# Kernel tuning notes

Hardware: AMD Instinct MI355X
Metric: run time of the kernel (lower is better)

The kernel has to match this reference:

```python
import jax, jax.numpy as jnp
import numpy as np

EPS = 1e-6  # RMSNorm eps


def rms_norm(x, w):
    var = jnp.mean(jnp.square(x), axis=-1, keepdims=True)
    return x * jax.lax.rsqrt(var + EPS) * w


def setup_inputs() -> dict:
    B, N, D, L = 16, 4096, 512, 64
    key = jax.random.key(0)
    ks = jax.random.split(key, 12)
    query = jax.random.normal(ks[0], (B, D), jnp.float32)
    tokens = jax.random.normal(ks[1], (B, N, D), jnp.float32)
    padding_mask = jax.random.bernoulli(ks[2], 0.3, (B, N))  # True = padded
    latents = jax.random.normal(ks[3], (L, D), jnp.float32) * 0.02
    s = D ** -0.5
    Wq = jax.random.uniform(ks[4], (D, D), jnp.float32, -s, s)
    bq = jax.random.uniform(ks[5], (D,), jnp.float32, -s, s)
    Wk = jax.random.uniform(ks[6], (D, D), jnp.float32, -s, s)
    bk = jax.random.uniform(ks[7], (D,), jnp.float32, -s, s)
    Wv = jax.random.uniform(ks[8], (D, D), jnp.float32, -s, s)
    bv = jax.random.uniform(ks[9], (D,), jnp.float32, -s, s)
    norm_w = jnp.ones((D,), jnp.float32)
    return {"query": query, "tokens": tokens, "padding_mask": padding_mask,
            "latents": latents, "Wq": Wq, "bq": bq, "Wk": Wk, "bk": bk,
            "Wv": Wv, "bv": bv, "norm_w": norm_w}


def reference(query, tokens, padding_mask, latents, Wq, bq, Wk, bk, Wv, bv, norm_w):
    D = query.shape[-1]
    L = latents.shape[0]
    score_scale = float(D) ** -0.5

    valid = (~padding_mask).astype(tokens.dtype)[..., None]          # [B,N,1]
    masked_tokens = tokens * valid                                    # [B,N,D]

    latent_query = latents[None] + (query @ Wq + bq)[:, None, :]      # [B,L,D]
    keys = masked_tokens @ Wk + bk                                    # [B,N,D]
    values = (masked_tokens @ Wv + bv) * valid                        # [B,N,D]

    scores = jnp.einsum('bld,bnd->bln', latent_query, keys) * score_scale
    all_padded = jnp.all(padding_mask, axis=1, keepdims=True)         # [B,1]
    # safe key padding mask: if a row is entirely padded, unmask it to keep softmax finite
    safe_mask = (padding_mask & ~all_padded)[:, None, :]              # [B,1,N]
    scores = jnp.where(safe_mask, jnp.finfo(scores.dtype).min, scores)
    weights = jax.nn.softmax(scores.astype(jnp.float32), axis=-1).astype(values.dtype)

    out = jnp.einsum('bln,bnd->bld', weights, values)                 # [B,L,D]
    out = rms_norm(out, norm_w)
    out = out * (~all_padded).astype(out.dtype)[..., None]
    latent_mask = jnp.broadcast_to(all_padded, (all_padded.shape[0], L))
    return out, latent_mask
```

## Files before the change

kernel.cpp:

```cpp
#include <hip/hip_runtime.h>
#include <hip/hip_bf16.h>
#include <math.h>

#define BB 16
#define NN_ 4096
#define DD 512
#define LL 64
#define SCALE 0.044194173824159216f
#define RMS_EPS 1e-6f
#define MASKVAL -3.0e38f
#define PSZ (BB * LL * DD)
#define ZCH 32

using bf16x8 = __attribute__((ext_vector_type(8))) short;
using f32x4  = __attribute__((ext_vector_type(4))) float;

__device__ __forceinline__ unsigned short f2bf(float x) {
    return __bfloat16_as_ushort(__float2bfloat16(x));
}

__global__ __launch_bounds__(256) void k_qproj(const float* __restrict__ query, const float* __restrict__ Wq,
                                               const float* __restrict__ bq, float* __restrict__ qproj) {
    const int b = blockIdx.y;
    const int dl = threadIdx.x & 63;
    const int d = (blockIdx.x << 6) + dl;
    const int wv = threadIdx.x >> 6;
    __shared__ float q[DD];
    __shared__ float red[4][64];
    for (int e = threadIdx.x; e < DD; e += 256) q[e] = query[b * DD + e];
    __syncthreads();
    float acc = 0.f;
    #pragma unroll 8
    for (int i = 0; i < 128; ++i) {
        const int e = (wv << 7) + i;
        acc += q[e] * Wq[(size_t)e * DD + d];
    }
    red[wv][dl] = acc;
    __syncthreads();
    if (threadIdx.x < 64) {
        const int dd = (blockIdx.x << 6) + threadIdx.x;
        qproj[(size_t)b * DD + dd] = red[0][threadIdx.x] + red[1][threadIdx.x] +
                                     red[2][threadIdx.x] + red[3][threadIdx.x] + bq[dd];
    }
}

__global__ __launch_bounds__(256) void k_lkqk(const float* __restrict__ latents, const float* __restrict__ qproj,
                                              const float* __restrict__ Wk, const float* __restrict__ bk,
                                              float* __restrict__ Lk, float* __restrict__ Qk,
                                              float* __restrict__ sbL, float* __restrict__ sbQ) {
    const int r = blockIdx.y;
    const int e0 = blockIdx.x << 6;
    const int tid = threadIdx.x;
    __shared__ float row[DD];
    const float* src = (r < LL) ? (latents + (size_t)r * DD) : (qproj + (size_t)(r - LL) * DD);
    for (int dd = tid; dd < DD; dd += 256) row[dd] = src[dd];
    __syncthreads();
    const int e = e0 + (tid >> 2);
    const int part = tid & 3;
    const float4* w4 = (const float4*)(Wk + (size_t)e * DD);
    const float4* r4 = (const float4*)row;
    float acc = 0.f;
    #pragma unroll 8
    for (int j = 0; j < 32; ++j) {
        const int d4 = part + (j << 2);
        const float4 w = w4[d4], rr = r4[d4];
        acc += w.x * rr.x + w.y * rr.y + w.z * rr.z + w.w * rr.w;
    }
    acc += __shfl_xor(acc, 1);
    acc += __shfl_xor(acc, 2);
    if (part == 0) {
        if (r < LL) Lk[(size_t)r * DD + e] = acc;
        else        Qk[(size_t)(r - LL) * DD + e] = acc;
    }
    if (blockIdx.x == 0 && tid < 64) {
        float p = 0.f;
        #pragma unroll
        for (int dd = tid; dd < DD; dd += 64) p += bk[dd] * row[dd];
        #pragma unroll
        for (int off = 32; off > 0; off >>= 1) p += __shfl_xor(p, off);
        if (tid == 0) { if (r < LL) sbL[r] = p; else sbQ[r - LL] = p; }
    }
}

__global__ __launch_bounds__(256) void k_lqbf(const float* __restrict__ Lk, const float* __restrict__ Qk,
                                              unsigned short* __restrict__ LQbf) {
    const int l = blockIdx.x, b = blockIdx.y;
    const int d = threadIdx.x << 1;
    const float2 lv = *(const float2*)&Lk[(size_t)l * DD + d];
    const float2 qv = *(const float2*)&Qk[(size_t)b * DD + d];
    const unsigned o = (unsigned)f2bf(lv.x + qv.x) | ((unsigned)f2bf(lv.y + qv.y) << 16);
    *(unsigned*)&LQbf[(size_t)((b << 6) + l) * DD + d] = o;
}

__global__ __launch_bounds__(512, 2) void k_flash(const float* __restrict__ tokens,
                                                  const unsigned short* __restrict__ LQbf,
                                                  const float* __restrict__ sbL, const float* __restrict__ sbQ,
                                                  const int* __restrict__ pmask,
                                                  _Float16* __restrict__ part,
                                                  float* __restrict__ mz, float* __restrict__ sz) {
    const int z = blockIdx.x, b = blockIdx.y;
    const int tid = threadIdx.x;
    const int lane = tid & 63, w = tid >> 6;
    const int r16 = lane & 15, kl = lane >> 4;

    __shared__ int sB[2][64][36];
    __shared__ unsigned short sP[64][72];
    __shared__ int sTw[8][64][20];
    __shared__ float s_mn[64], s_sum[64], s_rr[64];
    __shared__ float s_pmax[2][64], s_psum[2][64];

    const int lq = (w & 3) << 4;
    const int nq = (w >> 2) << 5;

    f32x4 acc[4][4];
    #pragma unroll
    for (int m = 0; m < 4; ++m)
        #pragma unroll
        for (int ef = 0; ef < 4; ++ef)
            acc[m][ef] = (f32x4){0.f, 0.f, 0.f, 0.f};

    if (tid < 64) { s_mn[tid] = MASKVAL; s_sum[tid] = 0.f; }

    const float sq = sbQ[b];
    const unsigned short* lqrow = &LQbf[(size_t)((b << 6) + lq + r16) * DD];
    float sbl[4];
    #pragma unroll
    for (int q = 0; q < 4; ++q) sbl[q] = sbL[lq + (kl << 2) + q];

    const int p1_pair = tid >> 4;
    const int p1_d4 = (tid & 15) << 2;
    const int e0w = w << 6;
    __syncthreads();

    for (int t = 0; t < 2; ++t) {
        const int n0 = (z << 7) + (t << 6);
        f32x4 accS[2];
        accS[0] = (f32x4){0.f, 0.f, 0.f, 0.f};
        accS[1] = (f32x4){0.f, 0.f, 0.f, 0.f};

        const float* tbase = &tokens[(size_t)((b << 12) + n0 + (p1_pair << 1)) * DD + p1_d4];
        float4 pf0 = *(const float4*)tbase;
        float4 pf1 = *(const float4*)(tbase + DD);
        #pragma unroll
        for (int s8 = 0; s8 < 8; ++s8) {
            const int cur = s8 & 1;
            {
                int2 w0, w1;
                w0.x = (int)((unsigned)f2bf(pf0.x) | ((unsigned)f2bf(pf0.y) << 16));
                w0.y = (int)((unsigned)f2bf(pf0.z) | ((unsigned)f2bf(pf0.w) << 16));
                w1.x = (int)((unsigned)f2bf(pf1.x) | ((unsigned)f2bf(pf1.y) << 16));
                w1.y = (int)((unsigned)f2bf(pf1.z) | ((unsigned)f2bf(pf1.w) << 16));
                *(int2*)&sB[cur][(p1_pair << 1)][p1_d4 >> 1] = w0;
                *(int2*)&sB[cur][(p1_pair << 1) + 1][p1_d4 >> 1] = w1;
            }
            if (s8 < 7) {
                pf0 = *(const float4*)(tbase + ((s8 + 1) << 6));
                pf1 = *(const float4*)(tbase + DD + ((s8 + 1) << 6));
            }
            __syncthreads();
            #pragma unroll
            for (int kk2 = 0; kk2 < 2; ++kk2) {
                const bf16x8 af = *(const bf16x8*)&lqrow[(s8 << 6) + (kk2 << 5) + (kl << 3)];
                #pragma unroll
                for (int nf = 0; nf < 2; ++nf) {
                    const bf16x8 bfr = *(const bf16x8*)&sB[cur][nq + (nf << 4) + r16][(kk2 << 4) + (kl << 2)];
                    accS[nf] = __builtin_amdgcn_mfma_f32_16x16x32_bf16(af, bfr, accS[nf], 0, 0, 0);
                }
            }
        }

        float sv[2][4], tm4[4];
        #pragma unroll
        for (int nf = 0; nf < 2; ++nf) {
            const int ncol = nq + (nf << 4) + r16;
            const int pm = pmask[(size_t)(b << 12) + n0 + ncol];
            #pragma unroll
            for (int q = 0; q < 4; ++q) {
                const float sval = (accS[nf][q] + sbl[q] + sq) * SCALE;
                sv[nf][q] = pm ? MASKVAL : sval;
            }
        }
        #pragma unroll
        for (int q = 0; q < 4; ++q) tm4[q] = fmaxf(sv[0][q], sv[1][q]);
        #pragma unroll
        for (int off = 1; off <= 8; off <<= 1)
            #pragma unroll
            for (int q = 0; q < 4; ++q) tm4[q] = fmaxf(tm4[q], __shfl_xor(tm4[q], off));
        if (r16 == 0) {
            #pragma unroll
            for (int q = 0; q < 4; ++q) s_pmax[w >> 2][lq + (kl << 2) + q] = tm4[q];
        }
        __syncthreads();
        if (tid < 64) {
            const float tmx = fmaxf(s_pmax[0][tid], s_pmax[1][tid]);
            const float mo = s_mn[tid];
            const float mn = fmaxf(mo, tmx);
            s_rr[tid] = __expf(mo - mn);
            s_mn[tid] = mn;
        }
        __syncthreads();
        float ps4[4];
        #pragma unroll
        for (int q = 0; q < 4; ++q) {
            const int l = lq + (kl << 2) + q;
            const float mn = s_mn[l];
            const float p0 = __expf(sv[0][q] - mn);
            const float p1 = __expf(sv[1][q] - mn);
            sP[l][nq + r16] = f2bf(p0);
            sP[l][nq + 16 + r16] = f2bf(p1);
            ps4[q] = p0 + p1;
        }
        #pragma unroll
        for (int off = 1; off <= 8; off <<= 1)
            #pragma unroll
            for (int q = 0; q < 4; ++q) ps4[q] += __shfl_xor(ps4[q], off);
        if (r16 == 0) {
            #pragma unroll
            for (int q = 0; q < 4; ++q) s_psum[w >> 2][lq + (kl << 2) + q] = ps4[q];
        }
        #pragma unroll
        for (int m = 0; m < 4; ++m) {
            #pragma unroll
            for (int q = 0; q < 4; ++q) {
                const float rrr = s_rr[(m << 4) + (kl << 2) + q];
                #pragma unroll
                for (int ef = 0; ef < 4; ++ef) acc[m][ef][q] *= rrr;
            }
        }
        __syncthreads();
        if (tid < 64) s_sum[tid] = s_sum[tid] * s_rr[tid] + s_psum[0][tid] + s_psum[1][tid];

        #pragma unroll
        for (int kk = 0; kk < 2; ++kk) {
            #pragma unroll
            for (int rep = 0; rep < 4; ++rep) {
                const int p = (lane >> 4) + (rep << 2);
                const int e4 = (lane & 15) << 2;
                const float* tp = &tokens[(size_t)((b << 12) + n0 + (kk << 5) + (p << 1)) * DD + e0w + e4];
                const float4 t0 = *(const float4*)tp;
                const float4 t1 = *(const float4*)(tp + DD);
                const float* a0 = (const float*)&t0;
                const float* a1 = (const float*)&t1;
                #pragma unroll
                for (int j = 0; j < 4; ++j) {
                    const int e = e4 + j;
                    const int col = p ^ (((((e >> 2) ^ (e >> 4))) & 3) << 2);
                    sTw[w][e][col] = (int)((unsigned)f2bf(a0[j]) | ((unsigned)f2bf(a1[j]) << 16));
                }
            }
            bf16x8 pa[4];
            #pragma unroll
            for (int m = 0; m < 4; ++m)
                pa[m] = *(const bf16x8*)&sP[(m << 4) + r16][(kk << 5) + (kl << 3)];
            #pragma unroll
            for (int ef = 0; ef < 4; ++ef) {
                const int e = (ef << 4) + r16;
                const int col4 = (kl << 2) ^ (((((e >> 2) ^ (e >> 4))) & 3) << 2);
                const bf16x8 bv = *(const bf16x8*)&sTw[w][e][col4];
                #pragma unroll
                for (int m = 0; m < 4; ++m)
                    acc[m][ef] = __builtin_amdgcn_mfma_f32_16x16x32_bf16(pa[m], bv, acc[m][ef], 0, 0, 0);
            }
        }
        __syncthreads();
    }

    #pragma unroll
    for (int m = 0; m < 4; ++m) {
        #pragma unroll
        for (int ef = 0; ef < 4; ++ef) {
            #pragma unroll
            for (int q = 0; q < 4; ++q) {
                const int l = (m << 4) + (kl << 2) + q;
                const int e = e0w + (ef << 4) + r16;
                part[(size_t)((z << 10) + (b << 6) + l) * DD + e] = (_Float16)acc[m][ef][q];
            }
        }
    }
    if (tid < 64) {
        mz[(z << 10) + (b << 6) + tid] = s_mn[tid];
        sz[(z << 10) + (b << 6) + tid] = s_sum[tid];
    }
}

__global__ __launch_bounds__(256) void k_combine(const _Float16* __restrict__ part,
                                                 const float* __restrict__ mz, const float* __restrict__ sz,
                                                 float* __restrict__ pacc, float* __restrict__ dmg) {
    const int row = blockIdx.x;
    const int t = threadIdx.x;
    float mg = MASKVAL;
    float mv[ZCH];
    #pragma unroll
    for (int zz = 0; zz < ZCH; ++zz) {
        mv[zz] = mz[(zz << 10) + row];
        mg = fmaxf(mg, mv[zz]);
    }
    float den = 0.f;
    float fz[ZCH];
    #pragma unroll
    for (int zz = 0; zz < ZCH; ++zz) {
        fz[zz] = __expf(mv[zz] - mg);
        den += sz[(zz << 10) + row] * fz[zz];
    }
    float a0 = 0.f, a1 = 0.f;
    #pragma unroll 8
    for (int zz = 0; zz < ZCH; ++zz) {
        const size_t base = (size_t)((zz << 10) + row) * DD;
        a0 += (float)part[base + t] * fz[zz];
        a1 += (float)part[base + t + 256] * fz[zz];
    }
    const float inv = 1.f / den;
    pacc[(size_t)row * DD + t] = a0 * inv;
    pacc[(size_t)row * DD + t + 256] = a1 * inv;
    if (t == 0) dmg[row] = mg;
}

__global__ __launch_bounds__(256) void k_proj(const float* __restrict__ pacc, const float* __restrict__ Wv,
                                              const float* __restrict__ bv, float* __restrict__ proj) {
    const int d0 = blockIdx.x * 64;
    const int r0 = blockIdx.y * 64;
    const int tid = threadIdx.x;
    const int rsub = (tid >> 4) << 2;
    const int dsub = (tid & 15) << 2;
    __shared__ float at[64][68];
    __shared__ float wv[64][68];
    float acc[4][4] = {{0.f, 0.f, 0.f, 0.f}};
    for (int kc = 0; kc < 8; ++kc) {
        const int k0 = kc * 64;
        for (int k = tid; k < 1024; k += 256) {
            const int rr = k >> 4, c4 = (k & 15) << 2;
            *(float4*)&at[rr][c4] = *(const float4*)&pacc[(size_t)(r0 + rr) * DD + k0 + c4];
            *(float4*)&wv[rr][c4] = *(const float4*)&Wv[(size_t)(k0 + rr) * DD + d0 + c4];
        }
        __syncthreads();
        #pragma unroll
        for (int n4 = 0; n4 < 16; ++n4) {
            float4 a4[4];
            #pragma unroll
            for (int i = 0; i < 4; ++i) a4[i] = *(const float4*)&at[rsub + i][n4 << 2];
            const float4 b0 = *(const float4*)&wv[(n4 << 2) + 0][dsub];
            const float4 b1 = *(const float4*)&wv[(n4 << 2) + 1][dsub];
            const float4 b2 = *(const float4*)&wv[(n4 << 2) + 2][dsub];
            const float4 b3 = *(const float4*)&wv[(n4 << 2) + 3][dsub];
            #pragma unroll
            for (int i = 0; i < 4; ++i) {
                const float4 av = a4[i];
                acc[i][0] += av.x * b0.x + av.y * b1.x + av.z * b2.x + av.w * b3.x;
                acc[i][1] += av.x * b0.y + av.y * b1.y + av.z * b2.y + av.w * b3.y;
                acc[i][2] += av.x * b0.z + av.y * b1.z + av.z * b2.z + av.w * b3.z;
                acc[i][3] += av.x * b0.w + av.y * b1.w + av.z * b2.w + av.w * b3.w;
            }
        }
        __syncthreads();
    }
    #pragma unroll
    for (int i = 0; i < 4; ++i) {
        const int d = d0 + dsub;
        float4 v;
        v.x = acc[i][0] + bv[d + 0];
        v.y = acc[i][1] + bv[d + 1];
        v.z = acc[i][2] + bv[d + 2];
        v.w = acc[i][3] + bv[d + 3];
        *(float4*)&proj[(size_t)(r0 + rsub + i) * DD + d] = v;
    }
}

__global__ __launch_bounds__(256) void k_rmsout(const float* __restrict__ proj, const float* __restrict__ norm_w,
                                                const float* __restrict__ dmg, float* __restrict__ out) {
    const int row = blockIdx.x;
    const int tid = threadIdx.x;
    __shared__ float red[256];
    const float* pr = proj + (size_t)row * DD;
    const float v0 = pr[tid], v1 = pr[tid + 256];
    red[tid] = v0 * v0 + v1 * v1;
    __syncthreads();
    for (int st = 128; st > 0; st >>= 1) {
        if (tid < st) red[tid] += red[tid + st];
        __syncthreads();
    }
    const float var = red[0] / (float)DD;
    const float r = 1.0f / sqrtf(var + RMS_EPS);
    const int ap = (dmg[row] < -1.0e38f) ? 1 : 0;
    const float msk = ap ? 0.f : 1.f;
    out[(size_t)row * DD + tid]       = v0 * r * norm_w[tid] * msk;
    out[(size_t)row * DD + tid + 256] = v1 * r * norm_w[tid + 256] * msk;
    if (tid == 0) out[(size_t)PSZ + row] = ap ? 1.f : 0.f;
}

extern "C" void kernel_launch(void* const* d_in, const int* in_sizes, int n_in,
                              void* d_out, int out_size, void* d_ws, size_t ws_size,
                              hipStream_t stream) {
    const float* query   = (const float*)d_in[0];
    const float* tokens  = (const float*)d_in[1];
    const int*   pmask   = (const int*)d_in[2];
    const float* latents = (const float*)d_in[3];
    const float* Wq = (const float*)d_in[4];
    const float* bq = (const float*)d_in[5];
    const float* Wk = (const float*)d_in[6];
    const float* bk = (const float*)d_in[7];
    const float* Wv = (const float*)d_in[8];
    const float* bv = (const float*)d_in[9];
    const float* nw = (const float*)d_in[10];

    float* ws = (float*)d_ws;
    float* dmg    = ws;
    float* mzv    = ws + 1024;
    float* szv    = ws + 33792;
    float* qproj  = ws + 66560;
    float* Lk     = ws + 74752;
    float* Qk     = ws + 107520;
    float* sbL    = ws + 115712;
    float* sbQ    = ws + 115776;
    unsigned short* LQbf = (unsigned short*)(ws + 115968);
    _Float16* part = (_Float16*)(ws + 115968 + 262144);
    float* pacc   = ws + 115968 + 262144 + 8388608;
    float* proj   = ws + 115968 + 262144 + 8388608 + 524288;
    float* out    = (float*)d_out;

    k_qproj<<<dim3(8, 16), 256, 0, stream>>>(query, Wq, bq, qproj);
    k_lkqk<<<dim3(8, 80), 256, 0, stream>>>(latents, qproj, Wk, bk, Lk, Qk, sbL, sbQ);
    k_lqbf<<<dim3(64, 16), 256, 0, stream>>>(Lk, Qk, LQbf);
    k_flash<<<dim3(ZCH, 16), 512, 0, stream>>>(tokens, LQbf, sbL, sbQ, pmask, part, mzv, szv);
    k_combine<<<1024, 256, 0, stream>>>(part, mzv, szv, pacc, dmg);
    k_proj<<<dim3(8, 16), 256, 0, stream>>>(pacc, Wv, bv, proj);
    k_rmsout<<<1024, 256, 0, stream>>>(proj, nw, dmg, out);
}
```

Baseline: 115.0 us.

## Split flash kernel over two output-column halves and deepen token prefetch

The flash kernel grid doubles so each block handles half of the D output columns, with the accumulator and shared transpose buffer halved. The score phase (the QK^T over the full D) is recomputed redundantly in both halves. The stage-1 token prefetch now holds four slices in registers instead of one, and uses an explicit waitcnt plus barrier. The combine kernel reads packed half pairs and writes float2. The aim is more parallelism and latency hiding, paid for with duplicated score work and extra token reads.

```diff
diff --git a/kernel.cpp b/kernel.cpp
--- a/kernel.cpp
+++ b/kernel.cpp
@@ -98,25 +98,27 @@
                                                   const int* __restrict__ pmask,
                                                   _Float16* __restrict__ part,
                                                   float* __restrict__ mz, float* __restrict__ sz) {
-    const int z = blockIdx.x, b = blockIdx.y;
+    const int z = blockIdx.x & 31;
+    const int eh = blockIdx.x >> 5;
+    const int b = blockIdx.y;
     const int tid = threadIdx.x;
     const int lane = tid & 63, w = tid >> 6;
     const int r16 = lane & 15, kl = lane >> 4;
 
     __shared__ int sB[2][64][36];
     __shared__ unsigned short sP[64][72];
-    __shared__ int sTw[8][64][20];
+    __shared__ int sTw[8][32][20];
     __shared__ float s_mn[64], s_sum[64], s_rr[64];
     __shared__ float s_pmax[2][64], s_psum[2][64];
 
     const int lq = (w & 3) << 4;
     const int nq = (w >> 2) << 5;
 
-    f32x4 acc[4][4];
+    f32x4 acc[4][2];
     #pragma unroll
     for (int m = 0; m < 4; ++m)
         #pragma unroll
-        for (int ef = 0; ef < 4; ++ef)
+        for (int ef = 0; ef < 2; ++ef)
             acc[m][ef] = (f32x4){0.f, 0.f, 0.f, 0.f};
 
     if (tid < 64) { s_mn[tid] = MASKVAL; s_sum[tid] = 0.f; }
@@ -129,7 +131,7 @@
 
     const int p1_pair = tid >> 4;
     const int p1_d4 = (tid & 15) << 2;
-    const int e0w = w << 6;
+    const int e0w = (eh << 8) + (w << 5);
     __syncthreads();
 
     for (int t = 0; t < 2; ++t) {
@@ -139,25 +141,31 @@
         accS[1] = (f32x4){0.f, 0.f, 0.f, 0.f};
 
         const float* tbase = &tokens[(size_t)((b << 12) + n0 + (p1_pair << 1)) * DD + p1_d4];
-        float4 pf0 = *(const float4*)tbase;
-        float4 pf1 = *(const float4*)(tbase + DD);
+        float4 R0[4], R1[4];
+        #pragma unroll
+        for (int s = 0; s < 4; ++s) {
+            R0[s] = *(const float4*)(tbase + (s << 6));
+            R1[s] = *(const float4*)(tbase + DD + (s << 6));
+        }
         #pragma unroll
         for (int s8 = 0; s8 < 8; ++s8) {
-            const int cur = s8 & 1;
+            const int cur = s8 & 1, slot = s8 & 3;
             {
                 int2 w0, w1;
-                w0.x = (int)((unsigned)f2bf(pf0.x) | ((unsigned)f2bf(pf0.y) << 16));
-                w0.y = (int)((unsigned)f2bf(pf0.z) | ((unsigned)f2bf(pf0.w) << 16));
-                w1.x = (int)((unsigned)f2bf(pf1.x) | ((unsigned)f2bf(pf1.y) << 16));
-                w1.y = (int)((unsigned)f2bf(pf1.z) | ((unsigned)f2bf(pf1.w) << 16));
+                w0.x = (int)((unsigned)f2bf(R0[slot].x) | ((unsigned)f2bf(R0[slot].y) << 16));
+                w0.y = (int)((unsigned)f2bf(R0[slot].z) | ((unsigned)f2bf(R0[slot].w) << 16));
+                w1.x = (int)((unsigned)f2bf(R1[slot].x) | ((unsigned)f2bf(R1[slot].y) << 16));
+                w1.y = (int)((unsigned)f2bf(R1[slot].z) | ((unsigned)f2bf(R1[slot].w) << 16));
                 *(int2*)&sB[cur][(p1_pair << 1)][p1_d4 >> 1] = w0;
                 *(int2*)&sB[cur][(p1_pair << 1) + 1][p1_d4 >> 1] = w1;
             }
-            if (s8 < 7) {
-                pf0 = *(const float4*)(tbase + ((s8 + 1) << 6));
-                pf1 = *(const float4*)(tbase + DD + ((s8 + 1) << 6));
-            }
-            __syncthreads();
+            if (s8 < 4) {
+                R0[slot] = *(const float4*)(tbase + ((s8 + 4) << 6));
+                R1[slot] = *(const float4*)(tbase + DD + ((s8 + 4) << 6));
+            }
+            asm volatile("s_waitcnt lgkmcnt(0)" ::: "memory");
+            __builtin_amdgcn_sched_barrier(0);
+            __builtin_amdgcn_s_barrier();
             #pragma unroll
             for (int kk2 = 0; kk2 < 2; ++kk2) {
                 const bf16x8 af = *(const bf16x8*)&lqrow[(s8 << 6) + (kk2 << 5) + (kl << 3)];
@@ -168,6 +176,7 @@
                 }
             }
         }
+        __syncthreads();
 
         float sv[2][4], tm4[4];
         #pragma unroll
@@ -224,7 +233,7 @@
             for (int q = 0; q < 4; ++q) {
                 const float rrr = s_rr[(m << 4) + (kl << 2) + q];
                 #pragma unroll
-                for (int ef = 0; ef < 4; ++ef) acc[m][ef][q] *= rrr;
+                for (int ef = 0; ef < 2; ++ef) acc[m][ef][q] *= rrr;
             }
         }
         __syncthreads();
@@ -232,15 +241,21 @@
 
         #pragma unroll
         for (int kk = 0; kk < 2; ++kk) {
-            #pragma unroll
-            for (int rep = 0; rep < 4; ++rep) {
-                const int p = (lane >> 4) + (rep << 2);
-                const int e4 = (lane & 15) << 2;
+            float4 T0[2], T1[2];
+            #pragma unroll
+            for (int rep = 0; rep < 2; ++rep) {
+                const int p = (lane >> 3) + (rep << 3);
+                const int e4 = (lane & 7) << 2;
                 const float* tp = &tokens[(size_t)((b << 12) + n0 + (kk << 5) + (p << 1)) * DD + e0w + e4];
-                const float4 t0 = *(const float4*)tp;
-                const float4 t1 = *(const float4*)(tp + DD);
-                const float* a0 = (const float*)&t0;
-                const float* a1 = (const float*)&t1;
+                T0[rep] = *(const float4*)tp;
+                T1[rep] = *(const float4*)(tp + DD);
+            }
+            #pragma unroll
+            for (int rep = 0; rep < 2; ++rep) {
+                const int p = (lane >> 3) + (rep << 3);
+                const int e4 = (lane & 7) << 2;
+                const float* a0 = (const float*)&T0[rep];
+                const float* a1 = (const float*)&T1[rep];
                 #pragma unroll
                 for (int j = 0; j < 4; ++j) {
                     const int e = e4 + j;
@@ -253,7 +268,7 @@
             for (int m = 0; m < 4; ++m)
                 pa[m] = *(const bf16x8*)&sP[(m << 4) + r16][(kk << 5) + (kl << 3)];
             #pragma unroll
-            for (int ef = 0; ef < 4; ++ef) {
+            for (int ef = 0; ef < 2; ++ef) {
                 const int e = (ef << 4) + r16;
                 const int col4 = (kl << 2) ^ (((((e >> 2) ^ (e >> 4))) & 3) << 2);
                 const bf16x8 bv = *(const bf16x8*)&sTw[w][e][col4];
@@ -268,7 +283,7 @@
     #pragma unroll
     for (int m = 0; m < 4; ++m) {
         #pragma unroll
-        for (int ef = 0; ef < 4; ++ef) {
+        for (int ef = 0; ef < 2; ++ef) {
             #pragma unroll
             for (int q = 0; q < 4; ++q) {
                 const int l = (m << 4) + (kl << 2) + q;
@@ -302,16 +317,21 @@
         fz[zz] = __expf(mv[zz] - mg);
         den += sz[(zz << 10) + row] * fz[zz];
     }
+    const unsigned* p32 = (const unsigned*)part;
+    const unsigned base32 = (unsigned)(row << 8) + t;
     float a0 = 0.f, a1 = 0.f;
     #pragma unroll 8
     for (int zz = 0; zz < ZCH; ++zz) {
-        const size_t base = (size_t)((zz << 10) + row) * DD;
-        a0 += (float)part[base + t] * fz[zz];
-        a1 += (float)part[base + t + 256] * fz[zz];
+        union { unsigned u; _Float16 h[2]; } v;
+        v.u = p32[((size_t)zz << 18) + base32];
+        a0 += (float)v.h[0] * fz[zz];
+        a1 += (float)v.h[1] * fz[zz];
     }
     const float inv = 1.f / den;
-    pacc[(size_t)row * DD + t] = a0 * inv;
-    pacc[(size_t)row * DD + t + 256] = a1 * inv;
+    float2 o;
+    o.x = a0 * inv;
+    o.y = a1 * inv;
+    *(float2*)&pacc[((size_t)row << 9) + (t << 1)] = o;
     if (t == 0) dmg[row] = mg;
 }
 
@@ -420,7 +440,7 @@
     k_qproj<<<dim3(8, 16), 256, 0, stream>>>(query, Wq, bq, qproj);
     k_lkqk<<<dim3(8, 80), 256, 0, stream>>>(latents, qproj, Wk, bk, Lk, Qk, sbL, sbQ);
     k_lqbf<<<dim3(64, 16), 256, 0, stream>>>(Lk, Qk, LQbf);
-    k_flash<<<dim3(ZCH, 16), 512, 0, stream>>>(tokens, LQbf, sbL, sbQ, pmask, part, mzv, szv);
+    k_flash<<<dim3(64, 16), 512, 0, stream>>>(tokens, LQbf, sbL, sbQ, pmask, part, mzv, szv);
     k_combine<<<1024, 256, 0, stream>>>(part, mzv, szv, pacc, dmg);
     k_proj<<<dim3(8, 16), 256, 0, stream>>>(pacc, Wv, bv, proj);
     k_rmsout<<<1024, 256, 0, stream>>>(proj, nw, dmg, out);
```

After: 136.6 us. +18.8%, slower.

## Stream token tiles into LDS via direct global-to-LDS loads, keep LQ in registers

Applied to the files above, without the earlier changes.

The score phase of the flash kernel now copies fp32 token tiles straight into a swizzled LDS buffer with global_load_lds and converts them to bf16 when building MFMA fragments. Previously each thread loaded, converted and stored them itself. The latent-query fragments are preloaded into registers once instead of being re-read from global memory every step. The PV phase splits the transposed-token staging into two halves to shrink LDS use, and the combine kernel reads packed half2 values with float2 stores. These changes aim to cut register and VALU staging work and global re-reads, at the cost of more registers (16 bf16x8) and larger fp32 LDS tiles.

```diff
diff --git a/kernel.cpp b/kernel.cpp
--- a/kernel.cpp
+++ b/kernel.cpp
@@ -17,6 +17,14 @@
 
 __device__ __forceinline__ unsigned short f2bf(float x) {
     return __bfloat16_as_ushort(__float2bfloat16(x));
+}
+
+__device__ __forceinline__ void gl_lds16(const float* g, char* lds_generic, int lds_byte_off) {
+    const int off = __builtin_amdgcn_readfirstlane(lds_byte_off);
+    __builtin_amdgcn_global_load_lds(
+        (const __attribute__((address_space(1))) unsigned*)(const void*)g,
+        (__attribute__((address_space(3))) unsigned*)(void*)(lds_generic + off),
+        16, 0, 0);
 }
 
 __global__ __launch_bounds__(256) void k_qproj(const float* __restrict__ query, const float* __restrict__ Wq,
@@ -103,15 +111,23 @@
     const int lane = tid & 63, w = tid >> 6;
     const int r16 = lane & 15, kl = lane >> 4;
 
-    __shared__ int sB[2][64][36];
+    __shared__ float sB[2][64][64];
     __shared__ unsigned short sP[64][72];
-    __shared__ int sTw[8][64][20];
+    __shared__ int sTw[8][32][20];
     __shared__ float s_mn[64], s_sum[64], s_rr[64];
     __shared__ float s_pmax[2][64], s_psum[2][64];
 
     const int lq = (w & 3) << 4;
     const int nq = (w >> 2) << 5;
 
+    bf16x8 afLQ[16];
+    {
+        const unsigned short* lqrow = &LQbf[(size_t)((b << 6) + lq + r16) * DD];
+        #pragma unroll
+        for (int f = 0; f < 16; ++f)
+            afLQ[f] = *(const bf16x8*)&lqrow[(f << 5) + (kl << 3)];
+    }
+
     f32x4 acc[4][4];
     #pragma unroll
     for (int m = 0; m < 4; ++m)
@@ -122,14 +138,16 @@
     if (tid < 64) { s_mn[tid] = MASKVAL; s_sum[tid] = 0.f; }
 
     const float sq = sbQ[b];
-    const unsigned short* lqrow = &LQbf[(size_t)((b << 6) + lq + r16) * DD];
     float sbl[4];
     #pragma unroll
     for (int q = 0; q < 4; ++q) sbl[q] = sbL[lq + (kl << 2) + q];
 
-    const int p1_pair = tid >> 4;
-    const int p1_d4 = (tid & 15) << 2;
+    const int rA = (w << 3) + (lane >> 4);
+    const int rB = rA + 4;
+    const int dbA = ((lane & 15) ^ (rA & 15)) << 2;
+    const int dbB = ((lane & 15) ^ (rB & 15)) << 2;
     const int e0w = w << 6;
+    char* sB_base = (char*)&sB[0][0][0];
     __syncthreads();
 
     for (int t = 0; t < 2; ++t) {
@@ -138,32 +156,37 @@
         accS[0] = (f32x4){0.f, 0.f, 0.f, 0.f};
         accS[1] = (f32x4){0.f, 0.f, 0.f, 0.f};
 
-        const float* tbase = &tokens[(size_t)((b << 12) + n0 + (p1_pair << 1)) * DD + p1_d4];
-        float4 pf0 = *(const float4*)tbase;
-        float4 pf1 = *(const float4*)(tbase + DD);
+        const size_t gb = (size_t)((b << 12) + n0);
+
+        gl_lds16(&tokens[(gb + rA) * DD + dbA], sB_base, ((w << 3) << 8));
+        gl_lds16(&tokens[(gb + rB) * DD + dbB], sB_base, (((w << 3) + 4) << 8));
+
         #pragma unroll
         for (int s8 = 0; s8 < 8; ++s8) {
             const int cur = s8 & 1;
-            {
-                int2 w0, w1;
-                w0.x = (int)((unsigned)f2bf(pf0.x) | ((unsigned)f2bf(pf0.y) << 16));
-                w0.y = (int)((unsigned)f2bf(pf0.z) | ((unsigned)f2bf(pf0.w) << 16));
-                w1.x = (int)((unsigned)f2bf(pf1.x) | ((unsigned)f2bf(pf1.y) << 16));
-                w1.y = (int)((unsigned)f2bf(pf1.z) | ((unsigned)f2bf(pf1.w) << 16));
-                *(int2*)&sB[cur][(p1_pair << 1)][p1_d4 >> 1] = w0;
-                *(int2*)&sB[cur][(p1_pair << 1) + 1][p1_d4 >> 1] = w1;
-            }
+            asm volatile("s_waitcnt vmcnt(0)" ::: "memory");
+            __builtin_amdgcn_s_barrier();
             if (s8 < 7) {
-                pf0 = *(const float4*)(tbase + ((s8 + 1) << 6));
-                pf1 = *(const float4*)(tbase + DD + ((s8 + 1) << 6));
-            }
-            __syncthreads();
+                const int nxt = (s8 + 1) & 1;
+                gl_lds16(&tokens[(gb + rA) * DD + ((s8 + 1) << 6) + dbA], sB_base,
+                         (nxt << 14) + ((w << 3) << 8));
+                gl_lds16(&tokens[(gb + rB) * DD + ((s8 + 1) << 6) + dbB], sB_base,
+                         (nxt << 14) + (((w << 3) + 4) << 8));
+            }
             #pragma unroll
             for (int kk2 = 0; kk2 < 2; ++kk2) {
-                const bf16x8 af = *(const bf16x8*)&lqrow[(s8 << 6) + (kk2 << 5) + (kl << 3)];
+                const bf16x8 af = afLQ[(s8 << 1) | kk2];
                 #pragma unroll
                 for (int nf = 0; nf < 2; ++nf) {
-                    const bf16x8 bfr = *(const bf16x8*)&sB[cur][nq + (nf << 4) + r16][(kk2 << 4) + (kl << 2)];
+                    const int n = nq + (nf << 4) + r16;
+                    const int lb = (kk2 << 3) + (kl << 1);
+                    const float4 f0 = *(const float4*)&sB[cur][n][(lb ^ r16) << 2];
+                    const float4 f1 = *(const float4*)&sB[cur][n][((lb + 1) ^ r16) << 2];
+                    bf16x8 bfr;
+                    bfr[0] = (short)f2bf(f0.x); bfr[1] = (short)f2bf(f0.y);
+                    bfr[2] = (short)f2bf(f0.z); bfr[3] = (short)f2bf(f0.w);
+                    bfr[4] = (short)f2bf(f1.x); bfr[5] = (short)f2bf(f1.y);
+                    bfr[6] = (short)f2bf(f1.z); bfr[7] = (short)f2bf(f1.w);
                     accS[nf] = __builtin_amdgcn_mfma_f32_16x16x32_bf16(af, bfr, accS[nf], 0, 0, 0);
                 }
             }
@@ -232,34 +255,39 @@
 
         #pragma unroll
         for (int kk = 0; kk < 2; ++kk) {
-            #pragma unroll
-            for (int rep = 0; rep < 4; ++rep) {
-                const int p = (lane >> 4) + (rep << 2);
-                const int e4 = (lane & 15) << 2;
-                const float* tp = &tokens[(size_t)((b << 12) + n0 + (kk << 5) + (p << 1)) * DD + e0w + e4];
-                const float4 t0 = *(const float4*)tp;
-                const float4 t1 = *(const float4*)(tp + DD);
-                const float* a0 = (const float*)&t0;
-                const float* a1 = (const float*)&t1;
-                #pragma unroll
-                for (int j = 0; j < 4; ++j) {
-                    const int e = e4 + j;
-                    const int col = p ^ (((((e >> 2) ^ (e >> 4))) & 3) << 2);
-                    sTw[w][e][col] = (int)((unsigned)f2bf(a0[j]) | ((unsigned)f2bf(a1[j]) << 16));
-                }
-            }
             bf16x8 pa[4];
             #pragma unroll
             for (int m = 0; m < 4; ++m)
                 pa[m] = *(const bf16x8*)&sP[(m << 4) + r16][(kk << 5) + (kl << 3)];
             #pragma unroll
-            for (int ef = 0; ef < 4; ++ef) {
-                const int e = (ef << 4) + r16;
-                const int col4 = (kl << 2) ^ (((((e >> 2) ^ (e >> 4))) & 3) << 2);
-                const bf16x8 bv = *(const bf16x8*)&sTw[w][e][col4];
+            for (int h = 0; h < 2; ++h) {
                 #pragma unroll
-                for (int m = 0; m < 4; ++m)
-                    acc[m][ef] = __builtin_amdgcn_mfma_f32_16x16x32_bf16(pa[m], bv, acc[m][ef], 0, 0, 0);
+                for (int rep = 0; rep < 2; ++rep) {
+                    const int p = (lane >> 3) + (rep << 3);
+                    const int e4 = (lane & 7) << 2;
+                    const float* tp = &tokens[(size_t)((b << 12) + n0 + (kk << 5) + (p << 1)) * DD
+                                              + e0w + (h << 5) + e4];
+                    const float4 t0 = *(const float4*)tp;
+                    const float4 t1 = *(const float4*)(tp + DD);
+                    const float* a0 = (const float*)&t0;
+                    const float* a1 = (const float*)&t1;
+                    #pragma unroll
+                    for (int j = 0; j < 4; ++j) {
+                        const int e = e4 + j;
+                        const int col = p ^ ((((e >> 2) ^ (e >> 4)) & 3) << 2);
+                        sTw[w][e][col] = (int)((unsigned)f2bf(a0[j]) | ((unsigned)f2bf(a1[j]) << 16));
+                    }
+                }
+                #pragma unroll
+                for (int ef2 = 0; ef2 < 2; ++ef2) {
+                    const int e = (ef2 << 4) + r16;
+                    const int col4 = (kl << 2) ^ ((((e >> 2) ^ (e >> 4)) & 3) << 2);
+                    const bf16x8 bv = *(const bf16x8*)&sTw[w][e][col4];
+                    const int ef = (h << 1) + ef2;
+                    #pragma unroll
+                    for (int m = 0; m < 4; ++m)
+                        acc[m][ef] = __builtin_amdgcn_mfma_f32_16x16x32_bf16(pa[m], bv, acc[m][ef], 0, 0, 0);
+                }
             }
         }
         __syncthreads();
@@ -302,16 +330,21 @@
         fz[zz] = __expf(mv[zz] - mg);
         den += sz[(zz << 10) + row] * fz[zz];
     }
+    const unsigned* p32 = (const unsigned*)part;
+    const unsigned base32 = (unsigned)(row << 8) + t;
     float a0 = 0.f, a1 = 0.f;
     #pragma unroll 8
     for (int zz = 0; zz < ZCH; ++zz) {
-        const size_t base = (size_t)((zz << 10) + row) * DD;
-        a0 += (float)part[base + t] * fz[zz];
-        a1 += (float)part[base + t + 256] * fz[zz];
+        union { unsigned u; _Float16 h[2]; } v;
+        v.u = p32[((size_t)zz << 18) + base32];
+        a0 += (float)v.h[0] * fz[zz];
+        a1 += (float)v.h[1] * fz[zz];
     }
     const float inv = 1.f / den;
-    pacc[(size_t)row * DD + t] = a0 * inv;
-    pacc[(size_t)row * DD + t + 256] = a1 * inv;
+    float2 o;
+    o.x = a0 * inv;
+    o.y = a1 * inv;
+    *(float2*)&pacc[((size_t)row << 9) + (t << 1)] = o;
     if (t == 0) dmg[row] = mg;
 }
 
```

After: 115.6 us. Within noise of the previous version (+0.5%).
